# Kernel tuning notes

Measured on AMD Instinct MI355X. Metric: run time of the kernel, lower is better.

Reference implementation:

```python
import jax, jax.numpy as jnp
import numpy as np

B, T, D, H = 1, 2048, 1024, 16
HS = D // H  # 64
FF = 4 * D   # 4096
EPS = 1e-6


def rmsnorm(x, w):
    xf = x.astype(jnp.float32)
    n = xf * jax.lax.rsqrt(jnp.mean(xf * xf, axis=-1, keepdims=True) + EPS)
    return n.astype(x.dtype) * w


def setup_inputs() -> dict:
    key = jax.random.key(0)
    ks = jax.random.split(key, 9)
    s = 0.02
    return {
        "x": jax.random.normal(ks[0], (B, T, D), jnp.float32),
        "Wq": jax.random.normal(ks[1], (H, D, HS), jnp.float32) * s,
        "Wk": jax.random.normal(ks[2], (H, D, HS), jnp.float32) * s,
        "Wv": jax.random.normal(ks[3], (H, D, HS), jnp.float32) * s,
        "Wproj": jax.random.normal(ks[4], (H * HS, D), jnp.float32) * s,
        "bproj": jnp.zeros((D,), jnp.float32),
        "W1": jax.random.normal(ks[5], (D, FF), jnp.float32) * s,
        "W2": jax.random.normal(ks[6], (FF, D), jnp.float32) * s,
        "g1": jnp.ones((D,), jnp.float32),
        "g2": jnp.ones((D,), jnp.float32),
    }


def reference(x, Wq, Wk, Wv, Wproj, bproj, W1, W2, g1, g2):
    # --- self attention on RMSNorm(x) ---
    xn = rmsnorm(x, g1)                                   # [B,T,D]
    q = jnp.einsum('btd,hds->bhts', xn, Wq)               # [B,H,T,hs]
    k = jnp.einsum('btd,hds->bhts', xn, Wk)
    v = jnp.einsum('btd,hds->bhts', xn, Wv)
    scale = HS ** -0.5
    wei = jnp.einsum('bhts,bhus->bhtu', q, k) * scale     # [B,H,T,T]
    causal = jnp.tril(jnp.ones((T, T), bool))
    wei = jnp.where(causal, wei, -jnp.inf)
    wei = jax.nn.softmax(wei, axis=-1)
    attn = jnp.einsum('bhtu,bhus->bhts', wei, v)          # [B,H,T,hs]
    attn = attn.transpose(0, 2, 1, 3).reshape(B, T, H * HS)
    sa = attn @ Wproj + bproj                             # [B,T,D]
    x = x + sa
    # --- SiLU FFN on RMSNorm(x) ---
    xn2 = rmsnorm(x, g2)
    h = jax.nn.silu(xn2 @ W1)                             # [B,T,4D]
    x = x + h @ W2
    return x
```

## Files before the change

kernel.cpp:

```cpp
#include <hip/hip_runtime.h>

typedef unsigned short u16;
typedef unsigned int u32;
typedef __attribute__((ext_vector_type(4))) float f32x4;
typedef __attribute__((ext_vector_type(8))) __bf16 bf16x8;

#define T_SEQ 2048
#define DMODEL 1024
#define NHEAD 16
#define HEADS 64
#define FFDIM 4096
#define MNQ 2097152l

__device__ __forceinline__ u16 f2bf(float f) {
  u32 u = __builtin_bit_cast(u32, f);
  u = u + 0x7FFFu + ((u >> 16) & 1u);
  return (u16)(u >> 16);
}

__global__ __launch_bounds__(256) void prep_k(
    const float* __restrict__ Wq, const float* __restrict__ Wk,
    const float* __restrict__ Wv, const float* __restrict__ Wproj,
    const float* __restrict__ W1, const float* __restrict__ W2,
    const float* __restrict__ x, const float* __restrict__ g1,
    u16* __restrict__ QKVwT, u16* __restrict__ WprojT,
    u16* __restrict__ W1T, u16* __restrict__ W2T, u16* __restrict__ xn1) {
  __shared__ u16 tile[64 * 66];
  __shared__ float wsum[4];
  int bid = blockIdx.x;
  int tid = threadIdx.x;
  if (bid >= 3072) {
    int row = bid - 3072;
    const float4* xr = (const float4*)(x + (long)row * DMODEL);
    float4 v = xr[tid];
    float ss = v.x * v.x + v.y * v.y + v.z * v.z + v.w * v.w;
#pragma unroll
    for (int off = 32; off >= 1; off >>= 1) ss += __shfl_xor(ss, off, 64);
    if ((tid & 63) == 0) wsum[tid >> 6] = ss;
    __syncthreads();
    float tot = wsum[0] + wsum[1] + wsum[2] + wsum[3];
    float rms = rsqrtf(tot * (1.0f / DMODEL) + 1e-6f);
    float4 gv = ((const float4*)g1)[tid];
    ushort4 o4 = make_ushort4(f2bf(v.x * rms * gv.x), f2bf(v.y * rms * gv.y),
                              f2bf(v.z * rms * gv.z), f2bf(v.w * rms * gv.w));
    ((ushort4*)(xn1 + (long)row * DMODEL))[tid] = o4;
    return;
  }
  const float* in;
  u16* out;
  long ldin, ldout;
  int r0, c0;
  if (bid < 768) {
    int z = bid >> 4, xi = bid & 15;
    int wsel = z >> 4, h = z & 15;
    in = (wsel == 0 ? Wq : (wsel == 1 ? Wk : Wv)) + (long)h * 65536;
    out = QKVwT + (long)wsel * 1048576 + (long)h * 65536;
    ldin = 64; ldout = 1024;
    r0 = xi * 64; c0 = 0;
  } else if (bid < 1024) {
    int b = bid - 768;
    in = Wproj; out = WprojT; ldin = 1024; ldout = 1024;
    r0 = (b >> 4) * 64; c0 = (b & 15) * 64;
  } else if (bid < 2048) {
    int b = bid - 1024;
    in = W1; out = W1T; ldin = 4096; ldout = 1024;
    r0 = (b & 15) * 64; c0 = (b >> 4) * 64;
  } else {
    int b = bid - 2048;
    in = W2; out = W2T; ldin = 1024; ldout = 4096;
    r0 = (b >> 4) * 64; c0 = (b & 15) * 64;
  }
#pragma unroll
  for (int p = 0; p < 16; ++p) {
    int idx = p * 256 + tid;
    int r = idx >> 6, c = idx & 63;
    tile[c * 66 + r] = f2bf(in[(long)(r0 + r) * ldin + c0 + c]);
  }
  __syncthreads();
#pragma unroll
  for (int p = 0; p < 16; ++p) {
    int idx = p * 256 + tid;
    int c = idx >> 6, r = idx & 63;
    out[(long)(c0 + c) * ldout + r0 + r] = tile[c * 66 + r];
  }
}

__global__ __launch_bounds__(256) void proj_rms_k(
    const float* __restrict__ p0, const float* __restrict__ p1,
    const float* __restrict__ bias, const float* __restrict__ resid,
    const float* __restrict__ g, float* __restrict__ x1,
    u16* __restrict__ xn2) {
  int row = blockIdx.x;
  int tid = threadIdx.x;
  long i = (long)row * DMODEL + tid * 4;
  float4 a = *(const float4*)(p0 + i);
  float4 b = *(const float4*)(p0 + MNQ + i);
  float4 c = *(const float4*)(p1 + i);
  float4 d = *(const float4*)(p1 + MNQ + i);
  float4 r = *(const float4*)(resid + i);
  float4 bi = *(const float4*)(bias + tid * 4);
  float4 v;
  v.x = a.x + b.x + c.x + d.x + r.x + bi.x;
  v.y = a.y + b.y + c.y + d.y + r.y + bi.y;
  v.z = a.z + b.z + c.z + d.z + r.z + bi.z;
  v.w = a.w + b.w + c.w + d.w + r.w + bi.w;
  *(float4*)(x1 + i) = v;
  float ss = v.x * v.x + v.y * v.y + v.z * v.z + v.w * v.w;
#pragma unroll
  for (int off = 32; off >= 1; off >>= 1) ss += __shfl_xor(ss, off, 64);
  __shared__ float wsum[4];
  if ((tid & 63) == 0) wsum[tid >> 6] = ss;
  __syncthreads();
  float tot = wsum[0] + wsum[1] + wsum[2] + wsum[3];
  float rms = rsqrtf(tot * (1.0f / DMODEL) + 1e-6f);
  float4 gv = ((const float4*)g)[tid];
  ushort4 o4 = make_ushort4(f2bf(v.x * rms * gv.x), f2bf(v.y * rms * gv.y),
                            f2bf(v.z * rms * gv.z), f2bf(v.w * rms * gv.w));
  ((ushort4*)(xn2 + (long)row * DMODEL))[tid] = o4;
}

template <int EPI>
__global__ __launch_bounds__(256, 4) void gemm_bt_k(
    const u16* __restrict__ A, const u16* __restrict__ Bt, int N, int K, int kc,
    u16* __restrict__ out16, u16* __restrict__ vt,
    float* __restrict__ p0, float* __restrict__ p1) {
  __shared__ __align__(16) u16 As[2][128 * 32];
  __shared__ __align__(16) u16 Bs[2][64 * 32];
  int tid = threadIdx.x;
  int w = tid >> 6, lane = tid & 63;
  int quad = lane >> 4, l15 = lane & 15;
  int m0 = blockIdx.x * 128, n0 = blockIdx.y * 64;
  int kz = blockIdx.z;
  int wr = w >> 1, wc = w & 1;

  f32x4 acc[4][2] = {};

  int srow = tid >> 2;
  int sch = (tid & 3) * 8;
  const u16* Ag = A + (long)(m0 + srow) * K + sch;
  const u16* Ag2 = Ag + (long)64 * K;
  const u16* Bg = Bt + (long)(n0 + srow) * K + sch;
  int wof = srow * 32 + sch;

  int kbeg = kz * kc, kend = kbeg + kc;

  uint4 ra0 = *(const uint4*)(Ag + kbeg);
  uint4 ra1 = *(const uint4*)(Ag2 + kbeg);
  uint4 rb0 = *(const uint4*)(Bg + kbeg);
  *(uint4*)(As[0] + wof) = ra0;
  *(uint4*)(As[0] + 64 * 32 + wof) = ra1;
  *(uint4*)(Bs[0] + wof) = rb0;
  __syncthreads();

  int buf = 0;
  for (int kb = kbeg; kb < kend; kb += 32) {
    bool more = (kb + 32 < kend);
    if (more) {
      ra0 = *(const uint4*)(Ag + kb + 32);
      ra1 = *(const uint4*)(Ag2 + kb + 32);
      rb0 = *(const uint4*)(Bg + kb + 32);
    }
    bf16x8 af[4], bfr[2];
#pragma unroll
    for (int mt = 0; mt < 4; ++mt)
      af[mt] = *(const bf16x8*)(As[buf] + (wr * 64 + mt * 16 + l15) * 32 + quad * 8);
#pragma unroll
    for (int nt = 0; nt < 2; ++nt)
      bfr[nt] = *(const bf16x8*)(Bs[buf] + (wc * 32 + nt * 16 + l15) * 32 + quad * 8);
#pragma unroll
    for (int mt = 0; mt < 4; ++mt)
#pragma unroll
      for (int nt = 0; nt < 2; ++nt)
        acc[mt][nt] = __builtin_amdgcn_mfma_f32_16x16x32_bf16(
            af[mt], bfr[nt], acc[mt][nt], 0, 0, 0);
    if (more) {
      int nb = buf ^ 1;
      *(uint4*)(As[nb] + wof) = ra0;
      *(uint4*)(As[nb] + 64 * 32 + wof) = ra1;
      *(uint4*)(Bs[nb] + wof) = rb0;
      __syncthreads();
    }
    buf ^= 1;
  }

  bool vblock = (EPI == 0) && (vt != nullptr) && (n0 >= 2048);
  float* pb = nullptr;
  if (EPI == 4) pb = (kz < 2 ? p0 : p1) + (long)(kz & 1) * MNQ;
#pragma unroll
  for (int mt = 0; mt < 4; ++mt)
#pragma unroll
    for (int nt = 0; nt < 2; ++nt) {
      int col = n0 + wc * 32 + nt * 16 + l15;
      if (EPI == 0 && vblock) {
        int s = col - 2048;
        int row0 = m0 + wr * 64 + mt * 16 + quad * 4;
        ushort4 pk = make_ushort4(f2bf(acc[mt][nt][0]), f2bf(acc[mt][nt][1]),
                                  f2bf(acc[mt][nt][2]), f2bf(acc[mt][nt][3]));
        *(ushort4*)(vt + (long)s * 2048 + row0) = pk;
        continue;
      }
#pragma unroll
      for (int r = 0; r < 4; ++r) {
        int row = m0 + wr * 64 + mt * 16 + quad * 4 + r;
        long idx = (long)row * N + col;
        float v = acc[mt][nt][r];
        if (EPI == 0) {
          out16[idx] = f2bf(v);
        } else if (EPI == 2) {
          out16[idx] = f2bf(v / (1.0f + __expf(-v)));
        } else if (EPI == 4) {
          pb[idx] = v;
        }
      }
    }
}

__global__ __launch_bounds__(256) void reduce_ffn2_k(
    const float* __restrict__ p0, const float* __restrict__ p1,
    const float* __restrict__ resid, float* __restrict__ out) {
  long i = ((long)blockIdx.x * 256 + threadIdx.x) * 4;
  float4 a = *(const float4*)(p0 + i);
  float4 b = *(const float4*)(p0 + MNQ + i);
  float4 c = *(const float4*)(p1 + i);
  float4 d = *(const float4*)(p1 + MNQ + i);
  float4 r = *(const float4*)(resid + i);
  float4 o;
  o.x = a.x + b.x + c.x + d.x + r.x;
  o.y = a.y + b.y + c.y + d.y + r.y;
  o.z = a.z + b.z + c.z + d.z + r.z;
  o.w = a.w + b.w + c.w + d.w + r.w;
  *(float4*)(out + i) = o;
}

#define LSTR 72
__global__ __launch_bounds__(256) void attn_part_k(const u16* __restrict__ QKV,
                                                   const u16* __restrict__ Vt,
                                                   u16* __restrict__ Opart,
                                                   float* __restrict__ lpart) {
  __shared__ __align__(16) u16 Qs[64 * LSTR];
  __shared__ __align__(16) u16 Ks[64 * LSTR];
  __shared__ __align__(16) u16 Vs[64 * LSTR];

  int tid = threadIdx.x;
  int w = tid >> 6, lane = tid & 63;
  int quad = lane >> 4, l15 = lane & 15;
  int h = blockIdx.y;

  int p = blockIdx.x;
  int bx = 0, acc0 = 0;
  while (true) {
    int n = (bx >> 3) + 1;
    if (p < acc0 + n) break;
    acc0 += n;
    ++bx;
  }
  int c = p - acc0;
  int t0 = bx * 64;
  int jstart = c * 8;
  int jend = min(jstart + 8, bx + 1);

#pragma unroll
  for (int pp = 0; pp < 2; ++pp) {
    int idx = pp * 256 + tid;
    int row = idx >> 3, cc = idx & 7;
    *(uint4*)(Qs + row * LSTR + cc * 8) =
        *(const uint4*)(QKV + (long)(t0 + row) * 3072 + h * 64 + cc * 8);
  }
  __syncthreads();
  bf16x8 aq[2];
#pragma unroll
  for (int ks = 0; ks < 2; ++ks)
    aq[ks] = *(const bf16x8*)(Qs + (w * 16 + l15) * LSTR + ks * 32 + quad * 8);

  f32x4 oacc[4] = {};
  float lsum[4] = {0.f, 0.f, 0.f, 0.f};

  u16* PsW = Qs + w * (16 * LSTR);

  for (int j = jstart; j < jend; ++j) {
    __syncthreads();
#pragma unroll
    for (int pp = 0; pp < 2; ++pp) {
      int idx = pp * 256 + tid;
      int row = idx >> 3, cc = idx & 7;
      *(uint4*)(Ks + row * LSTR + cc * 8) =
          *(const uint4*)(QKV + (long)(j * 64 + row) * 3072 + 1024 + h * 64 + cc * 8);
      *(uint4*)(Vs + row * LSTR + cc * 8) =
          *(const uint4*)(Vt + (long)h * (64 * 2048) + (long)row * 2048 + j * 64 + cc * 8);
    }
    __syncthreads();

    f32x4 sacc[4] = {};
#pragma unroll
    for (int ks = 0; ks < 2; ++ks)
#pragma unroll
      for (int nt = 0; nt < 4; ++nt) {
        bf16x8 bk = *(const bf16x8*)(Ks + (nt * 16 + l15) * LSTR + ks * 32 + quad * 8);
        sacc[nt] = __builtin_amdgcn_mfma_f32_16x16x32_bf16(aq[ks], bk, sacc[nt], 0, 0, 0);
      }

    bool boundary = (j == bx);
#pragma unroll
    for (int nt = 0; nt < 4; ++nt)
#pragma unroll
      for (int r = 0; r < 4; ++r) {
        float pv = exp2f(sacc[nt][r] * 0.18033688f);
        if (boundary) {
          int u = j * 64 + nt * 16 + l15;
          int q = t0 + w * 16 + quad * 4 + r;
          if (u > q) pv = 0.f;
        }
        lsum[r] += pv;
        PsW[(quad * 4 + r) * LSTR + nt * 16 + l15] = f2bf(pv);
      }
    asm volatile("s_waitcnt lgkmcnt(0)" ::: "memory");
#pragma unroll
    for (int ks = 0; ks < 2; ++ks) {
      bf16x8 pf = *(const bf16x8*)(PsW + l15 * LSTR + ks * 32 + quad * 8);
#pragma unroll
      for (int ct = 0; ct < 4; ++ct) {
        bf16x8 vf = *(const bf16x8*)(Vs + (ct * 16 + l15) * LSTR + ks * 32 + quad * 8);
        oacc[ct] = __builtin_amdgcn_mfma_f32_16x16x32_bf16(pf, vf, oacc[ct], 0, 0, 0);
      }
    }
  }

#pragma unroll
  for (int off = 8; off >= 1; off >>= 1)
#pragma unroll
    for (int r = 0; r < 4; ++r) lsum[r] += __shfl_xor(lsum[r], off, 64);

  long slot = (long)p * 16 + h;
  float inv[4];
#pragma unroll
  for (int r = 0; r < 4; ++r) inv[r] = 1.0f / lsum[r];
  u16* Ob = Opart + slot * 4096;
#pragma unroll
  for (int ct = 0; ct < 4; ++ct)
#pragma unroll
    for (int r = 0; r < 4; ++r)
      Ob[(w * 16 + quad * 4 + r) * 64 + ct * 16 + l15] = f2bf(oacc[ct][r] * inv[r]);
  if (l15 == 0) {
    float* lp = lpart + slot * 64;
#pragma unroll
    for (int r = 0; r < 4; ++r) lp[w * 16 + quad * 4 + r] = lsum[r];
  }
}

__global__ __launch_bounds__(256) void attn_combine_k(
    const u16* __restrict__ Opart, const float* __restrict__ lpart,
    u16* __restrict__ out) {
  int bx = blockIdx.x, h = blockIdx.y;
  int g = bx >> 3;
  int p0 = 4 * g * (g + 1) + (bx - 8 * g) * (g + 1);
  int nc = g + 1;
  int tid = threadIdx.x;
  int row = tid >> 2, c4 = (tid & 3) * 16;

  float lv[4];
  float wsum = 0.f;
  for (int cidx = 0; cidx < nc; ++cidx) {
    long slot = (long)(p0 + cidx) * 16 + h;
    lv[cidx] = lpart[slot * 64 + row];
    wsum += lv[cidx];
  }
  float rinv = 1.0f / wsum;

  float o[16];
#pragma unroll
  for (int i = 0; i < 16; ++i) o[i] = 0.f;
  for (int cidx = 0; cidx < nc; ++cidx) {
    float wc = lv[cidx] * rinv;
    const u16* Ob = Opart + ((long)(p0 + cidx) * 16 + h) * 4096 + row * 64 + c4;
    bf16x8 a = *(const bf16x8*)Ob;
    bf16x8 b = *(const bf16x8*)(Ob + 8);
#pragma unroll
    for (int i = 0; i < 8; ++i) {
      o[i] += wc * (float)a[i];
      o[8 + i] += wc * (float)b[i];
    }
  }
  u16 ob[16];
#pragma unroll
  for (int i = 0; i < 16; ++i) ob[i] = f2bf(o[i]);
  u16* op = out + (long)(bx * 64 + row) * 1024 + h * 64 + c4;
  *(uint4*)op = *(uint4*)ob;
  *(uint4*)(op + 8) = *(uint4*)(ob + 8);
}

extern "C" void kernel_launch(void* const* d_in, const int* in_sizes, int n_in,
                              void* d_out, int out_size, void* d_ws, size_t ws_size,
                              hipStream_t stream) {
  const float* x     = (const float*)d_in[0];
  const float* Wq    = (const float*)d_in[1];
  const float* Wk    = (const float*)d_in[2];
  const float* Wv    = (const float*)d_in[3];
  const float* Wproj = (const float*)d_in[4];
  const float* bproj = (const float*)d_in[5];
  const float* W1    = (const float*)d_in[6];
  const float* W2    = (const float*)d_in[7];
  const float* g1    = (const float*)d_in[8];
  const float* g2    = (const float*)d_in[9];

  char* ws = (char*)d_ws;
  u16* QKVwT  = (u16*)(ws);
  u16* WprojT = (u16*)(ws + (6ul << 20));
  u16* W1T    = (u16*)(ws + (8ul << 20));
  u16* W2T    = (u16*)(ws + (16ul << 20));
  u16* xn1    = (u16*)(ws + (24ul << 20));
  u16* QKVb   = (u16*)(ws + (28ul << 20));
  u16* VtB    = (u16*)(ws + (40ul << 20));
  u16* attn   = (u16*)(ws + (44ul << 20));
  float* x1   = (float*)(ws + (48ul << 20));
  u16* xn2    = (u16*)(ws + (56ul << 20));
  u16* hbuf   = (u16*)(ws + (60ul << 20));
  u16* Opart    = (u16*)(ws + (48ul << 20));
  float* lpart  = (float*)(ws + (58ul << 20));
  float* projp0 = (float*)(ws + (28ul << 20));
  float* projp1 = (float*)(ws + (60ul << 20));
  float* ffn2pA = (float*)(ws + (28ul << 20));
  float* ffn2pB = (float*)(ws);
  if (ws_size < (76ul << 20)) return;

  dim3 blk(256);

  prep_k<<<dim3(5120), blk, 0, stream>>>(
      Wq, Wk, Wv, Wproj, W1, W2, x, g1, QKVwT, WprojT, W1T, W2T, xn1);
  gemm_bt_k<0><<<dim3(16, 48, 1), blk, 0, stream>>>(
      xn1, QKVwT, 3072, 1024, 1024, QKVb, VtB, nullptr, nullptr);
  attn_part_k<<<dim3(80, 16), blk, 0, stream>>>(QKVb, VtB, Opart, lpart);
  attn_combine_k<<<dim3(32, 16), blk, 0, stream>>>(Opart, lpart, attn);
  gemm_bt_k<4><<<dim3(16, 16, 4), blk, 0, stream>>>(
      attn, WprojT, 1024, 1024, 256, nullptr, nullptr, projp0, projp1);
  proj_rms_k<<<dim3(2048), blk, 0, stream>>>(projp0, projp1, bproj, x, g2, x1, xn2);
  gemm_bt_k<2><<<dim3(16, 64, 1), blk, 0, stream>>>(
      xn2, W1T, 4096, 1024, 1024, hbuf, nullptr, nullptr, nullptr);
  gemm_bt_k<4><<<dim3(16, 16, 4), blk, 0, stream>>>(
      hbuf, W2T, 1024, 4096, 1024, nullptr, nullptr, ffn2pA, ffn2pB);
  reduce_ffn2_k<<<dim3(2048), blk, 0, stream>>>(ffn2pA, ffn2pB, x1, (float*)d_out);
}
```

Baseline: 262.4 us.

## Use direct global-to-LDS loads in GEMM, bf16 split-K partials, transposed attention scores

The GEMM kernel now stages A and B tiles with global_load_lds, which writes global memory straight into LDS and drops the register round-trip. Split-K partial results are stored as bf16 in one contiguous buffer rather than fp32, halving partial-sum write and read traffic in the proj/FFN2 reductions at some precision cost. The attention kernel swaps the MFMA operand order so each lane holds one query row's scores, which simplifies the row-sum reduction and allows packed P stores. The bf16 partials add rounding error to the residual sum.

```diff
diff --git a/kernel.cpp b/kernel.cpp
--- a/kernel.cpp
+++ b/kernel.cpp
@@ -16,6 +16,15 @@
   u32 u = __builtin_bit_cast(u32, f);
   u = u + 0x7FFFu + ((u >> 16) & 1u);
   return (u16)(u >> 16);
+}
+__device__ __forceinline__ float bf2f(u16 h) {
+  u32 u = ((u32)h) << 16;
+  return __builtin_bit_cast(float, u);
+}
+__device__ __forceinline__ void gload_lds16(const u16* g, u16* l) {
+  __builtin_amdgcn_global_load_lds(
+      (const __attribute__((address_space(1))) u32*)g,
+      (__attribute__((address_space(3))) u32*)l, 16, 0, 0);
 }
 
 __global__ __launch_bounds__(256) void prep_k(
@@ -86,24 +95,21 @@
 }
 
 __global__ __launch_bounds__(256) void proj_rms_k(
-    const float* __restrict__ p0, const float* __restrict__ p1,
-    const float* __restrict__ bias, const float* __restrict__ resid,
-    const float* __restrict__ g, float* __restrict__ x1,
-    u16* __restrict__ xn2) {
+    const u16* __restrict__ part, const float* __restrict__ bias,
+    const float* __restrict__ resid, const float* __restrict__ g,
+    float* __restrict__ x1, u16* __restrict__ xn2) {
   int row = blockIdx.x;
   int tid = threadIdx.x;
   long i = (long)row * DMODEL + tid * 4;
-  float4 a = *(const float4*)(p0 + i);
-  float4 b = *(const float4*)(p0 + MNQ + i);
-  float4 c = *(const float4*)(p1 + i);
-  float4 d = *(const float4*)(p1 + MNQ + i);
   float4 r = *(const float4*)(resid + i);
   float4 bi = *(const float4*)(bias + tid * 4);
   float4 v;
-  v.x = a.x + b.x + c.x + d.x + r.x + bi.x;
-  v.y = a.y + b.y + c.y + d.y + r.y + bi.y;
-  v.z = a.z + b.z + c.z + d.z + r.z + bi.z;
-  v.w = a.w + b.w + c.w + d.w + r.w + bi.w;
+  v.x = r.x + bi.x; v.y = r.y + bi.y; v.z = r.z + bi.z; v.w = r.w + bi.w;
+#pragma unroll
+  for (int z = 0; z < 4; ++z) {
+    ushort4 a = *(const ushort4*)(part + z * MNQ + i);
+    v.x += bf2f(a.x); v.y += bf2f(a.y); v.z += bf2f(a.z); v.w += bf2f(a.w);
+  }
   *(float4*)(x1 + i) = v;
   float ss = v.x * v.x + v.y * v.y + v.z * v.z + v.w * v.w;
 #pragma unroll
@@ -122,8 +128,7 @@
 template <int EPI>
 __global__ __launch_bounds__(256, 4) void gemm_bt_k(
     const u16* __restrict__ A, const u16* __restrict__ Bt, int N, int K, int kc,
-    u16* __restrict__ out16, u16* __restrict__ vt,
-    float* __restrict__ p0, float* __restrict__ p1) {
+    u16* __restrict__ out16, u16* __restrict__ vt, u16* __restrict__ part) {
   __shared__ __align__(16) u16 As[2][128 * 32];
   __shared__ __align__(16) u16 Bs[2][64 * 32];
   int tid = threadIdx.x;
@@ -135,30 +140,27 @@
 
   f32x4 acc[4][2] = {};
 
-  int srow = tid >> 2;
-  int sch = (tid & 3) * 8;
-  const u16* Ag = A + (long)(m0 + srow) * K + sch;
-  const u16* Ag2 = Ag + (long)64 * K;
-  const u16* Bg = Bt + (long)(n0 + srow) * K + sch;
-  int wof = srow * 32 + sch;
+  int lr = lane >> 2, lc = (lane & 3) * 8;
+  const u16* AgL = A + (long)(m0 + w * 32 + lr) * K + lc;
+  const u16* BgL = Bt + (long)(n0 + w * 16 + lr) * K + lc;
+  u16* AsW[2] = {As[0] + w * 1024, As[1] + w * 1024};
+  u16* BsW[2] = {Bs[0] + w * 512, Bs[1] + w * 512};
 
   int kbeg = kz * kc, kend = kbeg + kc;
 
-  uint4 ra0 = *(const uint4*)(Ag + kbeg);
-  uint4 ra1 = *(const uint4*)(Ag2 + kbeg);
-  uint4 rb0 = *(const uint4*)(Bg + kbeg);
-  *(uint4*)(As[0] + wof) = ra0;
-  *(uint4*)(As[0] + 64 * 32 + wof) = ra1;
-  *(uint4*)(Bs[0] + wof) = rb0;
+  gload_lds16(AgL + kbeg, AsW[0]);
+  gload_lds16(AgL + 16 * K + kbeg, AsW[0] + 512);
+  gload_lds16(BgL + kbeg, BsW[0]);
   __syncthreads();
 
   int buf = 0;
   for (int kb = kbeg; kb < kend; kb += 32) {
     bool more = (kb + 32 < kend);
     if (more) {
-      ra0 = *(const uint4*)(Ag + kb + 32);
-      ra1 = *(const uint4*)(Ag2 + kb + 32);
-      rb0 = *(const uint4*)(Bg + kb + 32);
+      int nb = buf ^ 1;
+      gload_lds16(AgL + kb + 32, AsW[nb]);
+      gload_lds16(AgL + 16 * K + kb + 32, AsW[nb] + 512);
+      gload_lds16(BgL + kb + 32, BsW[nb]);
     }
     bf16x8 af[4], bfr[2];
 #pragma unroll
@@ -173,19 +175,13 @@
       for (int nt = 0; nt < 2; ++nt)
         acc[mt][nt] = __builtin_amdgcn_mfma_f32_16x16x32_bf16(
             af[mt], bfr[nt], acc[mt][nt], 0, 0, 0);
-    if (more) {
-      int nb = buf ^ 1;
-      *(uint4*)(As[nb] + wof) = ra0;
-      *(uint4*)(As[nb] + 64 * 32 + wof) = ra1;
-      *(uint4*)(Bs[nb] + wof) = rb0;
-      __syncthreads();
-    }
+    if (more) __syncthreads();
     buf ^= 1;
   }
 
   bool vblock = (EPI == 0) && (vt != nullptr) && (n0 >= 2048);
-  float* pb = nullptr;
-  if (EPI == 4) pb = (kz < 2 ? p0 : p1) + (long)(kz & 1) * MNQ;
+  u16* pb = nullptr;
+  if (EPI == 4) pb = part + (long)kz * MNQ;
 #pragma unroll
   for (int mt = 0; mt < 4; ++mt)
 #pragma unroll
@@ -209,26 +205,23 @@
         } else if (EPI == 2) {
           out16[idx] = f2bf(v / (1.0f + __expf(-v)));
         } else if (EPI == 4) {
-          pb[idx] = v;
+          pb[idx] = f2bf(v);
         }
       }
     }
 }
 
 __global__ __launch_bounds__(256) void reduce_ffn2_k(
-    const float* __restrict__ p0, const float* __restrict__ p1,
-    const float* __restrict__ resid, float* __restrict__ out) {
+    const u16* __restrict__ part, const float* __restrict__ resid,
+    float* __restrict__ out) {
   long i = ((long)blockIdx.x * 256 + threadIdx.x) * 4;
-  float4 a = *(const float4*)(p0 + i);
-  float4 b = *(const float4*)(p0 + MNQ + i);
-  float4 c = *(const float4*)(p1 + i);
-  float4 d = *(const float4*)(p1 + MNQ + i);
   float4 r = *(const float4*)(resid + i);
-  float4 o;
-  o.x = a.x + b.x + c.x + d.x + r.x;
-  o.y = a.y + b.y + c.y + d.y + r.y;
-  o.z = a.z + b.z + c.z + d.z + r.z;
-  o.w = a.w + b.w + c.w + d.w + r.w;
+  float4 o = r;
+#pragma unroll
+  for (int z = 0; z < 4; ++z) {
+    ushort4 a = *(const ushort4*)(part + z * MNQ + i);
+    o.x += bf2f(a.x); o.y += bf2f(a.y); o.z += bf2f(a.z); o.w += bf2f(a.w);
+  }
   *(float4*)(out + i) = o;
 }
 
@@ -240,6 +233,7 @@
   __shared__ __align__(16) u16 Qs[64 * LSTR];
   __shared__ __align__(16) u16 Ks[64 * LSTR];
   __shared__ __align__(16) u16 Vs[64 * LSTR];
+  __shared__ float lbuf[64];
 
   int tid = threadIdx.x;
   int w = tid >> 6, lane = tid & 63;
@@ -273,7 +267,8 @@
     aq[ks] = *(const bf16x8*)(Qs + (w * 16 + l15) * LSTR + ks * 32 + quad * 8);
 
   f32x4 oacc[4] = {};
-  float lsum[4] = {0.f, 0.f, 0.f, 0.f};
+  float lsum = 0.f;
+  int qg = t0 + w * 16 + l15;
 
   u16* PsW = Qs + w * (16 * LSTR);
 
@@ -294,25 +289,28 @@
 #pragma unroll
     for (int ks = 0; ks < 2; ++ks)
 #pragma unroll
-      for (int nt = 0; nt < 4; ++nt) {
-        bf16x8 bk = *(const bf16x8*)(Ks + (nt * 16 + l15) * LSTR + ks * 32 + quad * 8);
-        sacc[nt] = __builtin_amdgcn_mfma_f32_16x16x32_bf16(aq[ks], bk, sacc[nt], 0, 0, 0);
+      for (int ut = 0; ut < 4; ++ut) {
+        bf16x8 kf = *(const bf16x8*)(Ks + (ut * 16 + l15) * LSTR + ks * 32 + quad * 8);
+        sacc[ut] = __builtin_amdgcn_mfma_f32_16x16x32_bf16(kf, aq[ks], sacc[ut], 0, 0, 0);
       }
 
     bool boundary = (j == bx);
 #pragma unroll
-    for (int nt = 0; nt < 4; ++nt)
+    for (int ut = 0; ut < 4; ++ut) {
+      float pv[4];
 #pragma unroll
       for (int r = 0; r < 4; ++r) {
-        float pv = exp2f(sacc[nt][r] * 0.18033688f);
+        float v = exp2f(sacc[ut][r] * 0.18033688f);
         if (boundary) {
-          int u = j * 64 + nt * 16 + l15;
-          int q = t0 + w * 16 + quad * 4 + r;
-          if (u > q) pv = 0.f;
+          int u = j * 64 + ut * 16 + quad * 4 + r;
+          if (u > qg) v = 0.f;
         }
-        lsum[r] += pv;
-        PsW[(quad * 4 + r) * LSTR + nt * 16 + l15] = f2bf(pv);
+        pv[r] = v;
+        lsum += v;
       }
+      ushort4 pk = make_ushort4(f2bf(pv[0]), f2bf(pv[1]), f2bf(pv[2]), f2bf(pv[3]));
+      *(ushort4*)(PsW + l15 * LSTR + ut * 16 + quad * 4) = pk;
+    }
     asm volatile("s_waitcnt lgkmcnt(0)" ::: "memory");
 #pragma unroll
     for (int ks = 0; ks < 2; ++ks) {
@@ -325,26 +323,22 @@
     }
   }
 
-#pragma unroll
-  for (int off = 8; off >= 1; off >>= 1)
-#pragma unroll
-    for (int r = 0; r < 4; ++r) lsum[r] += __shfl_xor(lsum[r], off, 64);
+  lsum += __shfl_xor(lsum, 16, 64);
+  lsum += __shfl_xor(lsum, 32, 64);
+  if (quad == 0) lbuf[w * 16 + l15] = 1.0f / lsum;
+  asm volatile("s_waitcnt lgkmcnt(0)" ::: "memory");
 
   long slot = (long)p * 16 + h;
   float inv[4];
 #pragma unroll
-  for (int r = 0; r < 4; ++r) inv[r] = 1.0f / lsum[r];
+  for (int r = 0; r < 4; ++r) inv[r] = lbuf[w * 16 + quad * 4 + r];
   u16* Ob = Opart + slot * 4096;
 #pragma unroll
   for (int ct = 0; ct < 4; ++ct)
 #pragma unroll
     for (int r = 0; r < 4; ++r)
       Ob[(w * 16 + quad * 4 + r) * 64 + ct * 16 + l15] = f2bf(oacc[ct][r] * inv[r]);
-  if (l15 == 0) {
-    float* lp = lpart + slot * 64;
-#pragma unroll
-    for (int r = 0; r < 4; ++r) lp[w * 16 + quad * 4 + r] = lsum[r];
-  }
+  if (quad == 0) lpart[slot * 64 + w * 16 + l15] = lsum;
 }
 
 __global__ __launch_bounds__(256) void attn_combine_k(
@@ -416,10 +410,8 @@
   u16* hbuf   = (u16*)(ws + (60ul << 20));
   u16* Opart    = (u16*)(ws + (48ul << 20));
   float* lpart  = (float*)(ws + (58ul << 20));
-  float* projp0 = (float*)(ws + (28ul << 20));
-  float* projp1 = (float*)(ws + (60ul << 20));
-  float* ffn2pA = (float*)(ws + (28ul << 20));
-  float* ffn2pB = (float*)(ws);
+  u16* projp    = (u16*)(ws + (28ul << 20));
+  u16* ffn2p    = (u16*)(ws + (28ul << 20));
   if (ws_size < (76ul << 20)) return;
 
   dim3 blk(256);
@@ -427,15 +419,15 @@
   prep_k<<<dim3(5120), blk, 0, stream>>>(
       Wq, Wk, Wv, Wproj, W1, W2, x, g1, QKVwT, WprojT, W1T, W2T, xn1);
   gemm_bt_k<0><<<dim3(16, 48, 1), blk, 0, stream>>>(
-      xn1, QKVwT, 3072, 1024, 1024, QKVb, VtB, nullptr, nullptr);
+      xn1, QKVwT, 3072, 1024, 1024, QKVb, VtB, nullptr);
   attn_part_k<<<dim3(80, 16), blk, 0, stream>>>(QKVb, VtB, Opart, lpart);
   attn_combine_k<<<dim3(32, 16), blk, 0, stream>>>(Opart, lpart, attn);
   gemm_bt_k<4><<<dim3(16, 16, 4), blk, 0, stream>>>(
-      attn, WprojT, 1024, 1024, 256, nullptr, nullptr, projp0, projp1);
-  proj_rms_k<<<dim3(2048), blk, 0, stream>>>(projp0, projp1, bproj, x, g2, x1, xn2);
+      attn, WprojT, 1024, 1024, 256, nullptr, nullptr, projp);
+  proj_rms_k<<<dim3(2048), blk, 0, stream>>>(projp, bproj, x, g2, x1, xn2);
   gemm_bt_k<2><<<dim3(16, 64, 1), blk, 0, stream>>>(
-      xn2, W1T, 4096, 1024, 1024, hbuf, nullptr, nullptr, nullptr);
+      xn2, W1T, 4096, 1024, 1024, hbuf, nullptr, nullptr);
   gemm_bt_k<4><<<dim3(16, 16, 4), blk, 0, stream>>>(
-      hbuf, W2T, 1024, 4096, 1024, nullptr, nullptr, ffn2pA, ffn2pB);
-  reduce_ffn2_k<<<dim3(2048), blk, 0, stream>>>(ffn2pA, ffn2pB, x1, (float*)d_out);
-}
+      hbuf, W2T, 1024, 4096, 1024, nullptr, nullptr, ffn2p);
+  reduce_ffn2_k<<<dim3(2048), blk, 0, stream>>>(ffn2p, x1, (float*)d_out);
+}
```

New measurement: 255.9 us. 2.5% less time.
